# Performance work log

Hardware: AMD Instinct MI355X
Metric: run time of the kernel (lower is better)

## Reference

```python
import jax, jax.numpy as jnp
import numpy as np

NUM_CLASS = 5
IN_SIZE = 4
OBS_LEN = 20
EMBED = 256
B = 2048
N = 64
NUM_MODES = 20
IN_DIM = IN_SIZE * OBS_LEN  # 80


def setup_inputs() -> dict:
    key = jax.random.key(0)
    ks = jax.random.split(key, 12)
    s = 1.0 / np.sqrt(IN_DIM)
    inp = {
        "obs": jax.random.normal(ks[0], (B, OBS_LEN, IN_SIZE), jnp.float32),
        "neis": jax.random.normal(ks[1], (B, N, OBS_LEN, IN_SIZE), jnp.float32),
        "self_labels": jax.random.randint(ks[2], (B,), 0, NUM_CLASS),
        "nei_labels": jax.random.randint(ks[3], (B, N), 0, NUM_CLASS + 1),
        "modes": jax.random.normal(ks[4], (NUM_CLASS, NUM_MODES, EMBED), jnp.float32),
        # per-class obs embedding (ModuleList of Linear(in_dim, embed))
        "obs_W": jax.random.uniform(ks[5], (NUM_CLASS, IN_DIM, EMBED), jnp.float32, -s, s),
        "obs_b": jax.random.uniform(ks[6], (NUM_CLASS, EMBED), jnp.float32, -s, s),
        # per-class neighbor embedding (num_class+1 Linears)
        "nei_W": jax.random.uniform(ks[7], (NUM_CLASS + 1, IN_DIM, EMBED), jnp.float32, -s, s),
        "nei_b": jax.random.uniform(ks[8], (NUM_CLASS + 1, EMBED), jnp.float32, -s, s),
        # mode embedding Linear(2*embed, embed)
        "mode_W": jax.random.uniform(ks[9], (2 * EMBED, EMBED), jnp.float32, -1.0 / np.sqrt(2 * EMBED), 1.0 / np.sqrt(2 * EMBED)),
        "mode_b": jax.random.uniform(ks[10], (EMBED,), jnp.float32, -1.0 / np.sqrt(2 * EMBED), 1.0 / np.sqrt(2 * EMBED)),
    }
    return inp


def reference(obs, neis, self_labels, nei_labels, modes, obs_W, obs_b, nei_W, nei_b, mode_W, mode_b):
    obs_f = obs.reshape(B, IN_DIM)            # [B, in_dim]
    neis_f = neis.reshape(B, N, IN_DIM)       # [B, N, in_dim]
    eps = jnp.float32(1e-4)

    # label-routed obs embedding: one-hot selects the per-class Linear
    oh_s = jax.nn.one_hot(self_labels, NUM_CLASS, dtype=obs.dtype)          # [B, C]
    x = jnp.einsum("bi,cio,bc->bo", obs_f, obs_W, oh_s) + obs_b[self_labels]  # [B, E]

    # elementwise reciprocal transform (class-independent, applied to every neighbor row)
    r = jnp.where(neis_f >= 0, 1.0 / (neis_f + eps), 1.0 / (neis_f - eps))   # [B, N, in_dim]

    # label-routed neighbor embedding over num_class+1 experts
    oh_n = jax.nn.one_hot(nei_labels, NUM_CLASS + 1, dtype=obs.dtype)        # [B, N, C+1]
    nei_feats = jnp.einsum("bni,cio,bnc->bno", r, nei_W, oh_n) + nei_b[nei_labels]  # [B, N, E]

    mode_feats = modes[self_labels]                                          # [B, M, E]
    x_tiled = jnp.broadcast_to(x[:, None, :], (B, NUM_MODES, EMBED))
    cat = jnp.concatenate([x_tiled, mode_feats], axis=-1)                    # [B, M, 2E]
    out = jnp.einsum("bmk,ko->bmo", cat, mode_W) + mode_b                    # [B, M, E]
    return (out, nei_feats)
```

## Files before the change

### kernel.cpp

```cpp
#include <hip/hip_runtime.h>

#define BATCH 2048
#define NNEI 64
#define IN_DIM 80
#define EMBED 256
#define NCLS 5
#define NMODES 20
#define NROWS (BATCH * NNEI)
#define NEXP (NCLS + 1)
#define TM 16
#define GRID2 512

typedef __attribute__((ext_vector_type(8))) short bf16x8;
typedef __attribute__((ext_vector_type(4))) float f32x4;
typedef __attribute__((ext_vector_type(4))) int i32x4;

__device__ inline unsigned short bf16_rne(float f) {
    unsigned u = __builtin_bit_cast(unsigned, f);
    unsigned r = (u + 0x7fffu + ((u >> 16) & 1u)) >> 16;
    return (unsigned short)r;
}
__device__ inline float bf16_to_f(unsigned short h) {
    unsigned u = ((unsigned)h) << 16;
    return __builtin_bit_cast(float, u);
}

__global__ void bin_rows(const int* __restrict__ nei_labels,
                         int* __restrict__ counts, int* __restrict__ lists) {
    __shared__ int lc[NEXP], lb[NEXP];
    int t = threadIdx.x;
    if (t < NEXP) lc[t] = 0;
    __syncthreads();
    int r = blockIdx.x * 256 + t;
    int c = nei_labels[r];
    int lpos = atomicAdd(&lc[c], 1);
    __syncthreads();
    if (t < NEXP) lb[t] = atomicAdd(&counts[t], lc[t]);
    __syncthreads();
    lists[(size_t)c * NROWS + lb[c] + lpos] = r;
}

__global__ void wfrag_prep(const float* __restrict__ nei_W, unsigned short* __restrict__ wfrag) {
    int e = blockIdx.x;
    int l = threadIdx.x;
    int part = e & 1;
    int cfg = (e >> 1) & 15;
    int ks = (e >> 5) % 3;
    int c = e / 96;
    int col = cfg * 16 + (l & 15);
    unsigned short v[8] __attribute__((aligned(16)));
    #pragma unroll
    for (int j = 0; j < 8; ++j) {
        int k = ks * 32 + ((l >> 4) * 8) + j;
        float w = (k < IN_DIM) ? nei_W[((size_t)c * IN_DIM + k) * EMBED + col] : 0.f;
        unsigned short h = bf16_rne(w);
        if (part == 0) v[j] = h;
        else v[j] = bf16_rne(w - bf16_to_f(h));
    }
    unsigned short* dst = wfrag + ((size_t)e * 64 + l) * 8;
    *reinterpret_cast<i32x4*>(dst) = *reinterpret_cast<const i32x4*>(v);
}

__global__ void mode_proj(const float* __restrict__ modes,
                          const float* __restrict__ mode_W,
                          const float* __restrict__ mode_b,
                          float* __restrict__ proj) {
    int cm = blockIdx.x;
    int o = threadIdx.x;
    const float* mv = modes + (size_t)cm * EMBED;
    float acc = mode_b[o];
    #pragma unroll 8
    for (int k = 0; k < EMBED; ++k)
        acc = fmaf(mv[k], mode_W[(size_t)(EMBED + k) * EMBED + o], acc);
    proj[(size_t)cm * EMBED + o] = acc;
}

#define BPB 4
__global__ __launch_bounds__(256, 2)
void obs_mode(const float* __restrict__ obs, const int* __restrict__ self_labels,
              const float* __restrict__ obs_W, const float* __restrict__ obs_b,
              const float* __restrict__ mode_W, const float* __restrict__ proj,
              float* __restrict__ out0) {
    int b0 = blockIdx.x * BPB;
    int o = threadIdx.x;
    __shared__ float obs_s[BPB][IN_DIM];
    __shared__ float x_s[BPB][EMBED];
    __shared__ int cls_s[BPB];

    for (int t = threadIdx.x; t < BPB * IN_DIM; t += 256) {
        int bb = t / IN_DIM, k = t % IN_DIM;
        obs_s[bb][k] = obs[(size_t)(b0 + bb) * IN_DIM + k];
    }
    if (threadIdx.x < BPB) cls_s[threadIdx.x] = self_labels[b0 + threadIdx.x];
    __syncthreads();

    int c[BPB];
    float xacc[BPB];
    #pragma unroll
    for (int bb = 0; bb < BPB; ++bb) {
        c[bb] = cls_s[bb];
        xacc[bb] = obs_b[c[bb] * EMBED + o];
    }
    #pragma unroll 4
    for (int k = 0; k < IN_DIM; ++k) {
        #pragma unroll
        for (int bb = 0; bb < BPB; ++bb)
            xacc[bb] = fmaf(obs_s[bb][k],
                            obs_W[(size_t)c[bb] * IN_DIM * EMBED + (size_t)k * EMBED + o],
                            xacc[bb]);
    }
    #pragma unroll
    for (int bb = 0; bb < BPB; ++bb) x_s[bb][o] = xacc[bb];
    __syncthreads();

    float tacc[BPB];
    #pragma unroll
    for (int bb = 0; bb < BPB; ++bb) tacc[bb] = 0.f;
    #pragma unroll 4
    for (int k = 0; k < EMBED; ++k) {
        float wv = mode_W[(size_t)k * EMBED + o];
        #pragma unroll
        for (int bb = 0; bb < BPB; ++bb)
            tacc[bb] = fmaf(x_s[bb][k], wv, tacc[bb]);
    }
    #pragma unroll
    for (int bb = 0; bb < BPB; ++bb) {
        const float* pj = proj + (size_t)c[bb] * NMODES * EMBED;
        float* op = out0 + (size_t)(b0 + bb) * NMODES * EMBED;
        for (int m = 0; m < NMODES; ++m)
            op[m * EMBED + o] = tacc[bb] + pj[m * EMBED + o];
    }
}

__global__ __launch_bounds__(256, 2)
void nei_gemv_mfma(const float* __restrict__ neis,
                   const unsigned short* __restrict__ wfrag,
                   const float* __restrict__ nei_b,
                   const int* __restrict__ counts,
                   const int* __restrict__ lists,
                   float* __restrict__ out_n) {
    const int b = blockIdx.x;
    const int c = (b * NEXP) / GRID2;
    const int cstart = (c * GRID2 + NEXP - 1) / NEXP;
    const int cend = ((c + 1) * GRID2 + NEXP - 1) / NEXP;
    const int blk = b - cstart;
    const int nblk = cend - cstart;
    const int cnt = counts[c];
    const int ntiles = (cnt + TM - 1) / TM;
    if (blk >= ntiles || cnt == 0) return;

    const int ch = threadIdx.x >> 6;
    const int l = threadIdx.x & 63;
    const int* mylist = lists + (size_t)c * NROWS;
    const int kc = (l >> 4) * 8;

    bf16x8 wh[3][4], wl[3][4];
    {
        const unsigned short* wb = wfrag + (size_t)c * 96 * 64 * 8;
        #pragma unroll
        for (int ks = 0; ks < 3; ++ks)
            #pragma unroll
            for (int cf = 0; cf < 4; ++cf) {
                size_t base = ((((size_t)ks * 16 + (ch * 4 + cf)) * 2) * 64 + l) * 8;
                wh[ks][cf] = *reinterpret_cast<const bf16x8*>(wb + base);
                wl[ks][cf] = *reinterpret_cast<const bf16x8*>(wb + base + 64 * 8);
            }
    }
    #pragma unroll
    for (int ks = 0; ks < 3; ++ks)
        #pragma unroll
        for (int cf = 0; cf < 4; ++cf) {
            i32x4 th = __builtin_bit_cast(i32x4, wh[ks][cf]);
            asm volatile("" : "+v"(th));
            wh[ks][cf] = __builtin_bit_cast(bf16x8, th);
            i32x4 tl = __builtin_bit_cast(i32x4, wl[ks][cf]);
            asm volatile("" : "+v"(tl));
            wl[ks][cf] = __builtin_bit_cast(bf16x8, tl);
        }

    float bias[4];
    #pragma unroll
    for (int cf = 0; cf < 4; ++cf) {
        bias[cf] = nei_b[c * EMBED + (ch * 4 + cf) * 16 + (l & 15)];
        asm volatile("" : "+v"(bias[cf]));
    }

#define LOADT(F, R, T) {                                                      \
    int gi_ = (T) * TM + (l & 15);                                            \
    R = mylist[min(gi_, cnt - 1)];                                            \
    const float* bp_ = neis + (size_t)(unsigned)R * IN_DIM;                   \
    _Pragma("unroll")                                                         \
    for (int ks_ = 0; ks_ < 3; ++ks_) {                                       \
        int k0_ = ks_ * 32 + kc;                                              \
        if (k0_ + 8 > IN_DIM) k0_ = 0;          \
        *reinterpret_cast<float4*>(&F[ks_ * 8])     = *reinterpret_cast<const float4*>(bp_ + k0_);     \
        *reinterpret_cast<float4*>(&F[ks_ * 8 + 4]) = *reinterpret_cast<const float4*>(bp_ + k0_ + 4); \
    } }

#define COMPT(F, R, T) {                                                      \
    bf16x8 ah_[3], al_[3];                                                    \
    _Pragma("unroll")                                                         \
    for (int ks_ = 0; ks_ < 3; ++ks_) {                                       \
        _Pragma("unroll")                                                     \
        for (int j_ = 0; j_ < 8; ++j_) {                                      \
            float v_ = F[ks_ * 8 + j_];                                       \
            float d_ = (v_ >= 0.f) ? (v_ + 1e-4f) : (v_ - 1e-4f);             \
            float r_ = __builtin_amdgcn_rcpf(d_);                             \
            unsigned short hi_ = bf16_rne(r_);                                \
            ah_[ks_][j_] = (short)hi_;                                        \
            al_[ks_][j_] = (short)bf16_rne(r_ - bf16_to_f(hi_));              \
        }                                                                     \
    }                                                                         \
    f32x4 acc_[4];                                                            \
    _Pragma("unroll")                                                         \
    for (int cf_ = 0; cf_ < 4; ++cf_) acc_[cf_] = (f32x4){0.f, 0.f, 0.f, 0.f};\
    _Pragma("unroll")                                                         \
    for (int ks_ = 0; ks_ < 3; ++ks_) {                                       \
        _Pragma("unroll")                                                     \
        for (int cf_ = 0; cf_ < 4; ++cf_) {                                   \
            acc_[cf_] = __builtin_amdgcn_mfma_f32_16x16x32_bf16(ah_[ks_], wh[ks_][cf_], acc_[cf_], 0, 0, 0); \
            acc_[cf_] = __builtin_amdgcn_mfma_f32_16x16x32_bf16(al_[ks_], wh[ks_][cf_], acc_[cf_], 0, 0, 0); \
            acc_[cf_] = __builtin_amdgcn_mfma_f32_16x16x32_bf16(ah_[ks_], wl[ks_][cf_], acc_[cf_], 0, 0, 0); \
        }                                                                     \
    }                                                                         \
    int rb_ = (l >> 4) * 4;                                                   \
    _Pragma("unroll")                                                         \
    for (int i_ = 0; i_ < 4; ++i_) {                                          \
        int rid_ = __shfl(R, rb_ + i_);                                       \
        if ((T) * TM + rb_ + i_ < cnt) {                                      \
            float* op_ = out_n + (size_t)(unsigned)rid_ * EMBED + (l & 15);   \
            _Pragma("unroll")                                                 \
            for (int cf_ = 0; cf_ < 4; ++cf_)                                 \
                op_[(ch * 4 + cf_) * 16] = acc_[cf_][i_] + bias[cf_];         \
        }                                                                     \
    } }

    float fA[24], fB[24];
    int ridA, ridB;
    int tile = blk;
    LOADT(fA, ridA, tile)
    while (true) {
        int nt = tile + nblk;
        bool hn = nt < ntiles;
        if (hn) LOADT(fB, ridB, nt)
        COMPT(fA, ridA, tile)
        if (!hn) break;
        tile = nt;
        nt = tile + nblk;
        hn = nt < ntiles;
        if (hn) LOADT(fA, ridA, nt)
        COMPT(fB, ridB, tile)
        if (!hn) break;
        tile = nt;
    }
#undef LOADT
#undef COMPT
}

extern "C" void kernel_launch(void* const* d_in, const int* in_sizes, int n_in,
                              void* d_out, int out_size, void* d_ws, size_t ws_size,
                              hipStream_t stream) {
    const float* obs         = (const float*)d_in[0];
    const float* neis        = (const float*)d_in[1];
    const int*   self_labels = (const int*)d_in[2];
    const int*   nei_labels  = (const int*)d_in[3];
    const float* modes       = (const float*)d_in[4];
    const float* obs_W       = (const float*)d_in[5];
    const float* obs_b       = (const float*)d_in[6];
    const float* nei_W       = (const float*)d_in[7];
    const float* nei_b       = (const float*)d_in[8];
    const float* mode_W      = (const float*)d_in[9];
    const float* mode_b      = (const float*)d_in[10];

    float* out0  = (float*)d_out;
    float* out_n = out0 + (size_t)BATCH * NMODES * EMBED;

    char* ws = (char*)d_ws;
    int* counts = (int*)ws;
    int* lists  = (int*)(ws + 256);
    float* proj = (float*)(ws + 256 + (size_t)NEXP * NROWS * 4);
    unsigned short* wfrag = (unsigned short*)(ws + 256 + (size_t)NEXP * NROWS * 4
                                              + (size_t)NCLS * NMODES * EMBED * 4);

    hipMemsetAsync(counts, 0, NEXP * sizeof(int), stream);

    bin_rows<<<NROWS / 256, 256, 0, stream>>>(nei_labels, counts, lists);
    wfrag_prep<<<NEXP * 96, 64, 0, stream>>>(nei_W, wfrag);
    mode_proj<<<NCLS * NMODES, 256, 0, stream>>>(modes, mode_W, mode_b, proj);
    obs_mode<<<BATCH / BPB, 256, 0, stream>>>(obs, self_labels, obs_W, obs_b,
                                              mode_W, proj, out0);
    nei_gemv_mfma<<<GRID2, 256, 0, stream>>>(neis, wfrag, nei_b,
                                             counts, lists, out_n);
}
```

Before: 105.6 us.

## Fuse prep kernels, stage row ids in LDS, triple-buffer neighbor loads

Merges the binning, weight-fragment and mode-projection kernels into one launch, with block ranges choosing the branch, to cut launch overhead. In the neighbor MFMA kernel, each block now loads all its tile row ids into shared memory up front. This takes the dependent list-index global load off the critical path of each neis fetch. The loop also moves from double to triple buffering so two tiles are in flight while one computes. The cost is more registers and shared memory per block, which may reduce occupancy.

```diff
diff --git a/kernel.cpp b/kernel.cpp
--- a/kernel.cpp
+++ b/kernel.cpp
@@ -10,6 +10,11 @@
 #define NEXP (NCLS + 1)
 #define TM 16
 #define GRID2 512
+#define MAXT 104
+
+#define NBIN (NROWS / 256)
+#define NWF 144
+#define NPRJ (NCLS * NMODES)
 
 typedef __attribute__((ext_vector_type(8))) short bf16x8;
 typedef __attribute__((ext_vector_type(4))) float f32x4;
@@ -25,54 +30,54 @@
     return __builtin_bit_cast(float, u);
 }
 
-__global__ void bin_rows(const int* __restrict__ nei_labels,
-                         int* __restrict__ counts, int* __restrict__ lists) {
+__global__ void prep_all(const int* __restrict__ nei_labels,
+                         int* __restrict__ counts, int* __restrict__ lists,
+                         const float* __restrict__ nei_W, unsigned short* __restrict__ wfrag,
+                         const float* __restrict__ modes, const float* __restrict__ mode_W,
+                         const float* __restrict__ mode_b, float* __restrict__ proj) {
     __shared__ int lc[NEXP], lb[NEXP];
-    int t = threadIdx.x;
-    if (t < NEXP) lc[t] = 0;
-    __syncthreads();
-    int r = blockIdx.x * 256 + t;
-    int c = nei_labels[r];
-    int lpos = atomicAdd(&lc[c], 1);
-    __syncthreads();
-    if (t < NEXP) lb[t] = atomicAdd(&counts[t], lc[t]);
-    __syncthreads();
-    lists[(size_t)c * NROWS + lb[c] + lpos] = r;
-}
-
-__global__ void wfrag_prep(const float* __restrict__ nei_W, unsigned short* __restrict__ wfrag) {
-    int e = blockIdx.x;
-    int l = threadIdx.x;
-    int part = e & 1;
-    int cfg = (e >> 1) & 15;
-    int ks = (e >> 5) % 3;
-    int c = e / 96;
-    int col = cfg * 16 + (l & 15);
-    unsigned short v[8] __attribute__((aligned(16)));
-    #pragma unroll
-    for (int j = 0; j < 8; ++j) {
-        int k = ks * 32 + ((l >> 4) * 8) + j;
-        float w = (k < IN_DIM) ? nei_W[((size_t)c * IN_DIM + k) * EMBED + col] : 0.f;
-        unsigned short h = bf16_rne(w);
-        if (part == 0) v[j] = h;
-        else v[j] = bf16_rne(w - bf16_to_f(h));
-    }
-    unsigned short* dst = wfrag + ((size_t)e * 64 + l) * 8;
-    *reinterpret_cast<i32x4*>(dst) = *reinterpret_cast<const i32x4*>(v);
-}
-
-__global__ void mode_proj(const float* __restrict__ modes,
-                          const float* __restrict__ mode_W,
-                          const float* __restrict__ mode_b,
-                          float* __restrict__ proj) {
-    int cm = blockIdx.x;
-    int o = threadIdx.x;
-    const float* mv = modes + (size_t)cm * EMBED;
-    float acc = mode_b[o];
-    #pragma unroll 8
-    for (int k = 0; k < EMBED; ++k)
-        acc = fmaf(mv[k], mode_W[(size_t)(EMBED + k) * EMBED + o], acc);
-    proj[(size_t)cm * EMBED + o] = acc;
+    const int b = blockIdx.x;
+    const int t = threadIdx.x;
+
+    if (b < NBIN) {
+        if (t < NEXP) lc[t] = 0;
+        __syncthreads();
+        int r = b * 256 + t;
+        int c = nei_labels[r];
+        int lpos = atomicAdd(&lc[c], 1);
+        __syncthreads();
+        if (t < NEXP) lb[t] = atomicAdd(&counts[t], lc[t]);
+        __syncthreads();
+        lists[(size_t)c * NROWS + lb[c] + lpos] = r;
+    } else if (b < NBIN + NWF) {
+        int e = (b - NBIN) * 4 + (t >> 6);
+        int l = t & 63;
+        int part = e & 1;
+        int cfg = (e >> 1) & 15;
+        int ks = (e >> 5) % 3;
+        int c = e / 96;
+        int col = cfg * 16 + (l & 15);
+        unsigned short v[8] __attribute__((aligned(16)));
+        #pragma unroll
+        for (int j = 0; j < 8; ++j) {
+            int k = ks * 32 + ((l >> 4) * 8) + j;
+            float w = (k < IN_DIM) ? nei_W[((size_t)c * IN_DIM + k) * EMBED + col] : 0.f;
+            unsigned short h = bf16_rne(w);
+            if (part == 0) v[j] = h;
+            else v[j] = bf16_rne(w - bf16_to_f(h));
+        }
+        unsigned short* dst = wfrag + ((size_t)e * 64 + l) * 8;
+        *reinterpret_cast<i32x4*>(dst) = *reinterpret_cast<const i32x4*>(v);
+    } else {
+        int cm = b - (NBIN + NWF);
+        int o = t;
+        const float* mv = modes + (size_t)cm * EMBED;
+        float acc = mode_b[o];
+        #pragma unroll 8
+        for (int k = 0; k < EMBED; ++k)
+            acc = fmaf(mv[k], mode_W[(size_t)(EMBED + k) * EMBED + o], acc);
+        proj[(size_t)cm * EMBED + o] = acc;
+    }
 }
 
 #define BPB 4
@@ -147,12 +152,22 @@
     const int nblk = cend - cstart;
     const int cnt = counts[c];
     const int ntiles = (cnt + TM - 1) / TM;
+
+    __shared__ int rids_s[MAXT * TM];
+
     if (blk >= ntiles || cnt == 0) return;
+    const int nt = min((ntiles - blk + nblk - 1) / nblk, MAXT);
 
     const int ch = threadIdx.x >> 6;
     const int l = threadIdx.x & 63;
     const int* mylist = lists + (size_t)c * NROWS;
     const int kc = (l >> 4) * 8;
+
+    for (int i = threadIdx.x; i < nt * TM; i += 256) {
+        int j = i >> 4, r = i & 15;
+        int gi = (blk + j * nblk) * TM + r;
+        rids_s[i] = mylist[min(gi, cnt - 1)];
+    }
 
     bf16x8 wh[3][4], wl[3][4];
     {
@@ -177,17 +192,16 @@
             asm volatile("" : "+v"(tl));
             wl[ks][cf] = __builtin_bit_cast(bf16x8, tl);
         }
-
     float bias[4];
     #pragma unroll
     for (int cf = 0; cf < 4; ++cf) {
         bias[cf] = nei_b[c * EMBED + (ch * 4 + cf) * 16 + (l & 15)];
         asm volatile("" : "+v"(bias[cf]));
     }
-
-#define LOADT(F, R, T) {                                                      \
-    int gi_ = (T) * TM + (l & 15);                                            \
-    R = mylist[min(gi_, cnt - 1)];                                            \
+    __syncthreads();
+
+#define LOADJ(F, R, J) {                                                      \
+    R = rids_s[(J) * TM + (l & 15)];                                          \
     const float* bp_ = neis + (size_t)(unsigned)R * IN_DIM;                   \
     _Pragma("unroll")                                                         \
     for (int ks_ = 0; ks_ < 3; ++ks_) {                                       \
@@ -197,7 +211,7 @@
         *reinterpret_cast<float4*>(&F[ks_ * 8 + 4]) = *reinterpret_cast<const float4*>(bp_ + k0_ + 4); \
     } }
 
-#define COMPT(F, R, T) {                                                      \
+#define COMPJ(F, R, J) {                                                      \
     bf16x8 ah_[3], al_[3];                                                    \
     _Pragma("unroll")                                                         \
     for (int ks_ = 0; ks_ < 3; ++ks_) {                                       \
@@ -224,10 +238,11 @@
         }                                                                     \
     }                                                                         \
     int rb_ = (l >> 4) * 4;                                                   \
+    int tbase_ = (blk + (J) * nblk) * TM;                                     \
     _Pragma("unroll")                                                         \
     for (int i_ = 0; i_ < 4; ++i_) {                                          \
         int rid_ = __shfl(R, rb_ + i_);                                       \
-        if ((T) * TM + rb_ + i_ < cnt) {                                      \
+        if (tbase_ + rb_ + i_ < cnt) {                                        \
             float* op_ = out_n + (size_t)(unsigned)rid_ * EMBED + (l & 15);   \
             _Pragma("unroll")                                                 \
             for (int cf_ = 0; cf_ < 4; ++cf_)                                 \
@@ -235,26 +250,25 @@
         }                                                                     \
     } }
 
-    float fA[24], fB[24];
-    int ridA, ridB;
-    int tile = blk;
-    LOADT(fA, ridA, tile)
+    float fA[24], fB[24], fC[24];
+    int ridA, ridB, ridC;
+    LOADJ(fA, ridA, 0)
+    if (nt > 1) LOADJ(fB, ridB, 1)
+    int j = 0;
     while (true) {
-        int nt = tile + nblk;
-        bool hn = nt < ntiles;
-        if (hn) LOADT(fB, ridB, nt)
-        COMPT(fA, ridA, tile)
-        if (!hn) break;
-        tile = nt;
-        nt = tile + nblk;
-        hn = nt < ntiles;
-        if (hn) LOADT(fA, ridA, nt)
-        COMPT(fB, ridB, tile)
-        if (!hn) break;
-        tile = nt;
-    }
-#undef LOADT
-#undef COMPT
+        if (j + 2 < nt) LOADJ(fC, ridC, j + 2)
+        COMPJ(fA, ridA, j)
+        if (j + 1 >= nt) break;
+        if (j + 3 < nt) LOADJ(fA, ridA, j + 3)
+        COMPJ(fB, ridB, j + 1)
+        if (j + 2 >= nt) break;
+        if (j + 4 < nt) LOADJ(fB, ridB, j + 4)
+        COMPJ(fC, ridC, j + 2)
+        if (j + 3 >= nt) break;
+        j += 3;
+    }
+#undef LOADJ
+#undef COMPJ
 }
 
 extern "C" void kernel_launch(void* const* d_in, const int* in_sizes, int n_in,
@@ -284,9 +298,9 @@
 
     hipMemsetAsync(counts, 0, NEXP * sizeof(int), stream);
 
-    bin_rows<<<NROWS / 256, 256, 0, stream>>>(nei_labels, counts, lists);
-    wfrag_prep<<<NEXP * 96, 64, 0, stream>>>(nei_W, wfrag);
-    mode_proj<<<NCLS * NMODES, 256, 0, stream>>>(modes, mode_W, mode_b, proj);
+    prep_all<<<NBIN + NWF + NPRJ, 256, 0, stream>>>(nei_labels, counts, lists,
+                                                    nei_W, wfrag,
+                                                    modes, mode_W, mode_b, proj);
     obs_mode<<<BATCH / BPB, 256, 0, stream>>>(obs, self_labels, obs_W, obs_b,
                                               mode_W, proj, out0);
     nei_gemv_mfma<<<GRID2, 256, 0, stream>>>(neis, wfrag, nei_b,
```

Result: faster. 96.85 us (-8.3%).
